# Kernel optimization log

Measured on AMD Instinct MI355X. Metric: run time of the kernel, lower is better.

Reference implementation:

```python
import jax, jax.numpy as jnp
import numpy as np
import math

B, S, D = 4, 4096, 1024
NUM_HEADS = 8  # hardcoded in the original via `// 8` and view(..., 8, head_dim)
HEAD_DIM = D // NUM_HEADS


def setup_inputs() -> dict:
    key = jax.random.key(0)
    ks = jax.random.split(key, 11)
    s = 1.0 / math.sqrt(D)
    inp = {
        "input_seq": jax.random.normal(ks[0], (B, S, D), dtype=jnp.float32),
        # Linear weights stored as [in, out] (y = x @ W + b), matching nn.Linear math
        "Wq": jax.random.uniform(ks[1], (D, D), jnp.float32, -s, s),
        "bq": jax.random.uniform(ks[2], (D,), jnp.float32, -s, s),
        "Wk": jax.random.uniform(ks[3], (D, D), jnp.float32, -s, s),
        "bk": jax.random.uniform(ks[4], (D,), jnp.float32, -s, s),
        "Wv": jax.random.uniform(ks[5], (D, D), jnp.float32, -s, s),
        "bv": jax.random.uniform(ks[6], (D,), jnp.float32, -s, s),
        "W1": jax.random.uniform(ks[7], (D, D), jnp.float32, -s, s),
        "b1": jax.random.uniform(ks[8], (D,), jnp.float32, -s, s),
        "W2": jax.random.uniform(ks[9], (D, D), jnp.float32, -s, s),
        "b2": jax.random.uniform(ks[10], (D,), jnp.float32, -s, s),
    }
    return inp


def reference(input_seq, Wq, bq, Wk, bk, Wv, bv, W1, b1, W2, b2):
    # QKV projections (query=key=input_seq in self-attention)
    q = input_seq @ Wq + bq  # [B,S,D]
    k = input_seq @ Wk + bk
    v = input_seq @ Wv + bv

    # Faithful to the original: view(B, S, 8, head_dim) with NO transpose,
    # so attention is computed over the 8 heads within each token position.
    q = q.reshape(B, S, NUM_HEADS, HEAD_DIM)
    k = k.reshape(B, S, NUM_HEADS, HEAD_DIM)
    v = v.reshape(B, S, NUM_HEADS, HEAD_DIM)

    # scores[b,s,h,t] = q[b,s,h,:] . k[b,s,t,:] / sqrt(head_dim)  -> [B,S,8,8]
    scores = jnp.einsum("bshd,bstd->bsht", q, k) / jnp.sqrt(jnp.float32(HEAD_DIM))
    # dropout on scores before softmax: identity at inference
    attn_weights = jax.nn.softmax(scores, axis=-1)  # [B,S,8,8]

    out = jnp.einsum("bsht,bstd->bshd", attn_weights, v).reshape(B, S, D)
    # dropout on attn_output: identity at inference

    # FFN: Linear -> ReLU -> Linear (no residual / layernorm in the original)
    ff = jnp.maximum(out @ W1 + b1, 0.0) @ W2 + b2
    return ff, attn_weights
```

## Files before the change

### kernel.cpp

```cpp
#include <hip/hip_runtime.h>
#include <hip/hip_bf16.h>


#define DI __device__ __forceinline__

typedef __bf16 bf16raw;
typedef bf16raw bf16x8 __attribute__((ext_vector_type(8)));
typedef float floatx4 __attribute__((ext_vector_type(4)));
typedef unsigned int uint32x4 __attribute__((ext_vector_type(4)));

DI unsigned short f2bf(float f) {
    __hip_bfloat16 h = __float2bfloat16(f);
    return *reinterpret_cast<unsigned short*>(&h);
}

DI void async16(unsigned short* lds, const unsigned short* g) {
    __builtin_amdgcn_global_load_lds(
        (const __attribute__((address_space(1))) void*)g,
        (__attribute__((address_space(3))) void*)lds,
        16, 0, 0);
}

DI unsigned ldsaddr(const void* p) {
    return (unsigned)(unsigned long long)
        (__attribute__((address_space(3))) const void*)p;
}

template <typename T> DI T cvt_out(float v);
template <> DI float cvt_out<float>(float v) { return v; }
template <> DI unsigned short cvt_out<unsigned short>(float v) { return f2bf(v); }

template <int I0, int J0>
DI void mfma16(floatx4 (&acc)[8][4], const uint32x4 (&af)[4][2],
               const uint32x4 (&bf)[2][2]) {
#pragma unroll
    for (int s = 0; s < 2; s++)
#pragma unroll
        for (int i = 0; i < 4; i++)
#pragma unroll
            for (int j = 0; j < 2; j++)
                acc[I0 + i][J0 + j] = __builtin_amdgcn_mfma_f32_16x16x32_bf16(
                    __builtin_bit_cast(bf16x8, af[i][s]),
                    __builtin_bit_cast(bf16x8, bf[j][s]),
                    acc[I0 + i][J0 + j], 0, 0, 0);
}

#define STG_A(b, rb, kt) do { \
    async16(&As[b][(rb) * 64 + wofs], aS + (size_t)(rb) * K + (kt)); \
    async16(&As[b][((rb) + 64) * 64 + wofs], aS + (size_t)((rb) + 64) * K + (kt)); \
} while (0)
#define STG_B(b, rb, kt) do { \
    async16(&Bs[b][(rb) * 64 + wofs], bS + (size_t)(rb) * K + (kt)); \
    async16(&Bs[b][((rb) + 64) * 64 + wofs], bS + (size_t)((rb) + 64) * K + (kt)); \
} while (0)

#define DSR(dst, va, offs) \
    asm volatile("ds_read_b128 %0, %1 offset:" offs : "=&v"(dst) : "v"(va))

#define LDA_LO(dst, va0, va1) do { \
    DSR(dst[0][0], va0, "0");     DSR(dst[0][1], va1, "0"); \
    DSR(dst[1][0], va0, "2048");  DSR(dst[1][1], va1, "2048"); \
    DSR(dst[2][0], va0, "4096");  DSR(dst[2][1], va1, "4096"); \
    DSR(dst[3][0], va0, "6144");  DSR(dst[3][1], va1, "6144"); \
} while (0)
#define LDA_HI(dst, va0, va1) do { \
    DSR(dst[0][0], va0, "16384"); DSR(dst[0][1], va1, "16384"); \
    DSR(dst[1][0], va0, "18432"); DSR(dst[1][1], va1, "18432"); \
    DSR(dst[2][0], va0, "20480"); DSR(dst[2][1], va1, "20480"); \
    DSR(dst[3][0], va0, "22528"); DSR(dst[3][1], va1, "22528"); \
} while (0)
#define LDB_LO(dst, va0, va1) do { \
    DSR(dst[0][0], va0, "0");     DSR(dst[0][1], va1, "0"); \
    DSR(dst[1][0], va0, "2048");  DSR(dst[1][1], va1, "2048"); \
} while (0)
#define LDB_HI(dst, va0, va1) do { \
    DSR(dst[0][0], va0, "16384"); DSR(dst[0][1], va1, "16384"); \
    DSR(dst[1][0], va0, "18432"); DSR(dst[1][1], va1, "18432"); \
} while (0)

#define BARRIER do { __builtin_amdgcn_s_barrier(); \
    __builtin_amdgcn_sched_barrier(0); } while (0)
#define LGKM(n) do { asm volatile("s_waitcnt lgkmcnt(" #n ")" ::: "memory"); \
    __builtin_amdgcn_sched_barrier(0); } while (0)
#define GATE4 asm volatile("s_waitcnt vmcnt(4)" ::: "memory")
#define PRIO1 __builtin_amdgcn_s_setprio(1)
#define PRIO0 __builtin_amdgcn_s_setprio(0)

template <int K, int N, int GX, typename OutT, bool RELU>
__global__ __launch_bounds__(512, 2)
void gemm256_bt(const unsigned short* __restrict__ A,
                const unsigned short* __restrict__ Bt,
                const float* __restrict__ bias,
                OutT* __restrict__ C)
{
    constexpr int BK = 64;
    constexpr int NT = K / BK;
    constexpr int NP = NT / 2;
    static_assert(NT % 2 == 0 && N % 256 == 0, "");

    __shared__ unsigned short As[2][256 * BK];
    __shared__ unsigned short Bs[2][256 * BK];

    const int tid  = threadIdx.x;
    const int wave = tid >> 6;
    const int lane = tid & 63;
    const int quad = lane >> 4;
    const int l16  = lane & 15;
    const int sw7  = l16 & 7;
    const int wm   = wave >> 2;
    const int wn   = wave & 3;

    const int g   = blockIdx.x + GX * blockIdx.y;
    const int xcd = g & 7;
    const int t   = g >> 3;
    const int bx  = t % GX;
    const int by  = t / GX + (gridDim.y >> 3) * xcd;
    const int m0  = by * 256;
    const int n0  = bx * 256;

    const int srow = tid >> 3;
    const int soct = ((tid & 7) ^ (srow & 7)) * 8;
    const unsigned short* aS = A  + (size_t)(m0 + srow) * K + soct;
    const unsigned short* bS = Bt + (size_t)(n0 + srow) * K + soct;
    const int wofs = wave * 512;

    const int aroB = (wm * 64 + l16) * 128;
    const int broB = (wn * 32 + l16) * 128;
    const int s0B  = (quad ^ sw7) * 16;
    const int s1B  = ((quad + 4) ^ sw7) * 16;
    const unsigned vaA0_0 = ldsaddr(&As[0][0]) + aroB + s0B;
    const unsigned vaA0_1 = ldsaddr(&As[0][0]) + aroB + s1B;
    const unsigned vaA1_0 = ldsaddr(&As[1][0]) + aroB + s0B;
    const unsigned vaA1_1 = ldsaddr(&As[1][0]) + aroB + s1B;
    const unsigned vaB0_0 = ldsaddr(&Bs[0][0]) + broB + s0B;
    const unsigned vaB0_1 = ldsaddr(&Bs[0][0]) + broB + s1B;
    const unsigned vaB1_0 = ldsaddr(&Bs[1][0]) + broB + s0B;
    const unsigned vaB1_1 = ldsaddr(&Bs[1][0]) + broB + s1B;

    floatx4 acc[8][4];
    const floatx4 zero = {0.f, 0.f, 0.f, 0.f};
#pragma unroll
    for (int i = 0; i < 8; i++)
#pragma unroll
        for (int j = 0; j < 4; j++) acc[i][j] = zero;

    uint32x4 aL[4][2], aH[4][2], bL[2][2], bH[2][2];

    STG_A(0, 0, 0); STG_B(0, 0, 0); STG_B(0, 128, 0); STG_A(0, 128, 0);
    STG_A(1, 0, BK); STG_B(1, 0, BK); STG_B(1, 128, BK); STG_A(1, 128, BK);
    asm volatile("s_waitcnt vmcnt(8)" ::: "memory");
    BARRIER;
    LDA_LO(aL, vaA0_0, vaA0_1);
    LDB_LO(bL, vaB0_0, vaB0_1);
    LGKM(0);

#pragma unroll 1
    for (int it = 0; it < NP; ++it) {
        const int kt2 = ((2 * it + 2) < NT ? (2 * it + 2) : (NT - 1)) * BK;
        const int kt3 = ((2 * it + 3) < NT ? (2 * it + 3) : (NT - 1)) * BK;

        BARRIER;
        LDB_HI(bH, vaB0_0, vaB0_1);
        STG_A(0, 0, kt2);
        LGKM(4);
        PRIO1; mfma16<0, 0>(acc, aL, bL); PRIO0;

        BARRIER;
        LDA_HI(aH, vaA0_0, vaA0_1);
        STG_B(0, 0, kt2);
        LGKM(8);
        PRIO1; mfma16<0, 2>(acc, aL, bH); PRIO0;

        GATE4;
        BARRIER;
        LDA_LO(aL, vaA1_0, vaA1_1);
        STG_B(0, 128, kt2);
        LGKM(8);
        PRIO1; mfma16<4, 0>(acc, aH, bL); PRIO0;

        BARRIER;
        LDB_LO(bL, vaB1_0, vaB1_1);
        STG_A(0, 128, kt2);
        LGKM(4);
        PRIO1; mfma16<4, 2>(acc, aH, bH); PRIO0;

        BARRIER;
        LDB_HI(bH, vaB1_0, vaB1_1);
        STG_A(1, 0, kt3);
        LGKM(4);
        PRIO1; mfma16<0, 0>(acc, aL, bL); PRIO0;

        BARRIER;
        LDA_HI(aH, vaA1_0, vaA1_1);
        STG_B(1, 0, kt3);
        LGKM(8);
        PRIO1; mfma16<0, 2>(acc, aL, bH); PRIO0;

        GATE4;
        BARRIER;
        LDA_LO(aL, vaA0_0, vaA0_1);
        STG_B(1, 128, kt3);
        LGKM(8);
        PRIO1; mfma16<4, 0>(acc, aH, bL); PRIO0;

        BARRIER;
        LDB_LO(bL, vaB0_0, vaB0_1);
        STG_A(1, 128, kt3);
        LGKM(4);
        PRIO1; mfma16<4, 2>(acc, aH, bH); PRIO0;
    }
    asm volatile("s_waitcnt vmcnt(0) lgkmcnt(0)" ::: "memory");
    __builtin_amdgcn_sched_barrier(0);

#pragma unroll
    for (int j = 0; j < 4; j++) {
        const int col = n0 + wn * 32 + (j & 1) * 16 + (j >> 1) * 128 + l16;
        const float bv = bias[col];
#pragma unroll
        for (int i = 0; i < 8; i++) {
            const int rb = m0 + wm * 64 + (i & 3) * 16 + (i >> 2) * 128 + quad * 4;
#pragma unroll
            for (int r = 0; r < 4; r++) {
                float v = acc[i][j][r] + bv;
                if (RELU) v = fmaxf(v, 0.f);
                C[(size_t)(rb + r) * N + col] = cvt_out<OutT>(v);
            }
        }
    }
}

#undef STG_A
#undef STG_B
#undef DSR
#undef LDA_LO
#undef LDA_HI
#undef LDB_LO
#undef LDB_HI
#undef BARRIER
#undef LGKM
#undef GATE4
#undef PRIO1
#undef PRIO0

__global__ void cast_f32_to_bf16(const float* __restrict__ src,
                                 unsigned short* __restrict__ dst, int n4) {
    int i = blockIdx.x * blockDim.x + threadIdx.x;
    if (i < n4) {
        float4 v = reinterpret_cast<const float4*>(src)[i];
        ushort4 o = { f2bf(v.x), f2bf(v.y), f2bf(v.z), f2bf(v.w) };
        reinterpret_cast<ushort4*>(dst)[i] = o;
    }
}

struct WPack {
    const float* src[5];
    unsigned short* dst[5];
};
__global__ void transpose_cast_all(WPack p) {
    __shared__ float tile[32][33];
    const float* W = p.src[blockIdx.z];
    unsigned short* Wt = p.dst[blockIdx.z];
    const int n0 = blockIdx.x * 32, k0 = blockIdx.y * 32;
    const int tx = threadIdx.x, ty = threadIdx.y;
#pragma unroll
    for (int i = 0; i < 32; i += 8)
        tile[ty + i][tx] = W[(size_t)(k0 + ty + i) * 1024 + n0 + tx];
    __syncthreads();
#pragma unroll
    for (int i = 0; i < 32; i += 8)
        Wt[(size_t)(n0 + ty + i) * 1024 + k0 + tx] = f2bf(tile[tx][ty + i]);
}

__global__ void concat_bias(const float* __restrict__ bq,
                            const float* __restrict__ bk,
                            const float* __restrict__ bv,
                            float* __restrict__ dst) {
    int i = blockIdx.x * blockDim.x + threadIdx.x;
    const float* s = (i < 1024) ? bq : ((i < 2048) ? bk : bv);
    dst[i] = s[i & 1023];
}

DI float dot8(unsigned a, unsigned b, float acc) {
    union { unsigned u; float f; } al, ah, bl, bh;
    al.u = a << 16; ah.u = a & 0xffff0000u;
    bl.u = b << 16; bh.u = b & 0xffff0000u;
    return acc + al.f * bl.f + ah.f * bh.f;
}

__global__ __launch_bounds__(256)
void attention_kernel(const unsigned short* __restrict__ qkv,
                      unsigned short* __restrict__ out_bf,
                      float* __restrict__ attn_w)
{
    __shared__ unsigned short sqkv[4][3072];
    __shared__ float sw[4][64];
    const int tid  = threadIdx.x;
    const int wave = tid >> 6;
    const int lane = tid & 63;
    const int m    = blockIdx.x * 4 + wave;

    {
        const uint4* src = reinterpret_cast<const uint4*>(qkv + (size_t)m * 3072);
        uint4* dst = reinterpret_cast<uint4*>(&sqkv[wave][0]);
#pragma unroll
        for (int i = 0; i < 6; i++) dst[lane + 64 * i] = src[lane + 64 * i];
    }
    __syncthreads();

    {
        const int h = lane >> 3, t = lane & 7;
        const uint2* q8 = reinterpret_cast<const uint2*>(&sqkv[wave][h * 128]);
        const uint2* k8 = reinterpret_cast<const uint2*>(&sqkv[wave][1024 + t * 128]);
        float dot = 0.f;
#pragma unroll
        for (int d = 0; d < 32; d++) {
            uint2 a = q8[d], b = k8[d];
            dot = dot8(a.x, b.x, dot);
            dot = dot8(a.y, b.y, dot);
        }
        float score = dot * 0.08838834764831843f;
        float mx = score;
#pragma unroll
        for (int o = 1; o < 8; o <<= 1) mx = fmaxf(mx, __shfl_xor(mx, o, 8));
        float e = __expf(score - mx);
        float sum = e;
#pragma unroll
        for (int o = 1; o < 8; o <<= 1) sum += __shfl_xor(sum, o, 8);
        float w = e / sum;
        sw[wave][lane] = w;
        attn_w[(size_t)m * 64 + lane] = w;
    }
    __syncthreads();

    {
        const int h  = lane >> 3;
        const int d0 = (lane & 7) * 16;
        float acc[16];
#pragma unroll
        for (int i = 0; i < 16; i++) acc[i] = 0.f;
#pragma unroll
        for (int t = 0; t < 8; t++) {
            const float w = sw[wave][h * 8 + t];
            const uint4* v8 = reinterpret_cast<const uint4*>(
                &sqkv[wave][2048 + t * 128 + d0]);
            uint4 v0 = v8[0], v1 = v8[1];
            unsigned vv[8] = { v0.x, v0.y, v0.z, v0.w, v1.x, v1.y, v1.z, v1.w };
#pragma unroll
            for (int i = 0; i < 8; i++) {
                union { unsigned u; float f; } lo, hi;
                lo.u = vv[i] << 16; hi.u = vv[i] & 0xffff0000u;
                acc[i * 2]     += w * lo.f;
                acc[i * 2 + 1] += w * hi.f;
            }
        }
        unsigned o[8];
#pragma unroll
        for (int i = 0; i < 8; i++)
            o[i] = (unsigned)f2bf(acc[i * 2]) | ((unsigned)f2bf(acc[i * 2 + 1]) << 16);
        uint4* dst = reinterpret_cast<uint4*>(out_bf + (size_t)m * 1024 + lane * 16);
        dst[0] = make_uint4(o[0], o[1], o[2], o[3]);
        dst[1] = make_uint4(o[4], o[5], o[6], o[7]);
    }
}

extern "C" void kernel_launch(void* const* d_in, const int* in_sizes, int n_in,
                              void* d_out, int out_size, void* d_ws, size_t ws_size,
                              hipStream_t stream) {
    const float* x  = (const float*)d_in[0];
    const float* Wq = (const float*)d_in[1];
    const float* bq = (const float*)d_in[2];
    const float* Wk = (const float*)d_in[3];
    const float* bk = (const float*)d_in[4];
    const float* Wv = (const float*)d_in[5];
    const float* bv = (const float*)d_in[6];
    const float* W1 = (const float*)d_in[7];
    const float* b1 = (const float*)d_in[8];
    const float* W2 = (const float*)d_in[9];
    const float* b2 = (const float*)d_in[10];

    constexpr int D = 1024;
    constexpr int M = 4 * 4096;
    constexpr size_t XN = (size_t)M * D;

    float* ff_out   = (float*)d_out;
    float* attn_out = (float*)d_out + XN;

    char* ws = (char*)d_ws;
    size_t off = 0;
    auto alloc = [&](size_t bytes) -> char* {
        char* p = ws + off;
        off += (bytes + 255) & ~(size_t)255;
        return p;
    };
    unsigned short* Xbf   = (unsigned short*)alloc(XN * 2);
    unsigned short* Wtqkv = (unsigned short*)alloc((size_t)3 * D * D * 2);
    unsigned short* Wt1   = (unsigned short*)alloc((size_t)D * D * 2);
    unsigned short* Wt2   = (unsigned short*)alloc((size_t)D * D * 2);
    float*          bqkv  = (float*)alloc(3 * D * 4);
    unsigned short* outbf = (unsigned short*)alloc(XN * 2);
    unsigned short* hbf   = (unsigned short*)alloc(XN * 2);
    unsigned short* qkv   = (unsigned short*)alloc((size_t)M * 3 * D * 2);

    cast_f32_to_bf16<<<(int)(XN / 4 / 256), 256, 0, stream>>>(x, Xbf, (int)(XN / 4));
    WPack p;
    p.src[0] = Wq; p.dst[0] = Wtqkv;
    p.src[1] = Wk; p.dst[1] = Wtqkv + (size_t)D * D;
    p.src[2] = Wv; p.dst[2] = Wtqkv + (size_t)2 * D * D;
    p.src[3] = W1; p.dst[3] = Wt1;
    p.src[4] = W2; p.dst[4] = Wt2;
    transpose_cast_all<<<dim3(32, 32, 5), dim3(32, 8), 0, stream>>>(p);
    concat_bias<<<12, 256, 0, stream>>>(bq, bk, bv, bqkv);

    gemm256_bt<D, 3 * D, 12, unsigned short, false>
        <<<dim3(12, 64), 512, 0, stream>>>(Xbf, Wtqkv, bqkv, qkv);
    attention_kernel<<<M / 4, 256, 0, stream>>>(qkv, outbf, attn_out);

    gemm256_bt<D, D, 4, unsigned short, true>
        <<<dim3(4, 64), 512, 0, stream>>>(outbf, Wt1, b1, hbf);
    gemm256_bt<D, D, 4, float, false>
        <<<dim3(4, 64), 512, 0, stream>>>(hbf, Wt2, b2, ff_out);
}
```

Before: 364.2 us.

## Restructure GEMM main loop with two barriers per phase and full LDS waits

Rewrites the software pipeline of the 256x256 bf16 GEMM main loop. Each phase now issues an LDS fragment read plus one global-to-LDS stage, waits for all LDS reads before its MFMA block, and then gates on vmcnt(12) with a second barrier. The earlier partial lgkmcnt waits and the single vmcnt(4) gate per half are gone, and stage issue order and the prologue change with them. The aim is a more regular hazard-safe schedule, but doubling the barriers and using full lgkm waits may cut the overlap between memory traffic and MFMA work.

After: 371.6 us. 1.02x slower.

```diff
diff --git a/kernel.cpp b/kernel.cpp
--- a/kernel.cpp
+++ b/kernel.cpp
@@ -78,11 +78,10 @@
     DSR(dst[1][0], va0, "18432"); DSR(dst[1][1], va1, "18432"); \
 } while (0)
 
-#define BARRIER do { __builtin_amdgcn_s_barrier(); \
-    __builtin_amdgcn_sched_barrier(0); } while (0)
-#define LGKM(n) do { asm volatile("s_waitcnt lgkmcnt(" #n ")" ::: "memory"); \
-    __builtin_amdgcn_sched_barrier(0); } while (0)
-#define GATE4 asm volatile("s_waitcnt vmcnt(4)" ::: "memory")
+#define SBAR __builtin_amdgcn_sched_barrier(0)
+#define BAR do { __builtin_amdgcn_s_barrier(); SBAR; } while (0)
+#define LGKM0 do { asm volatile("s_waitcnt lgkmcnt(0)" ::: "memory"); SBAR; } while (0)
+#define GATE12 do { asm volatile("s_waitcnt vmcnt(12)" ::: "memory"); SBAR; } while (0)
 #define PRIO1 __builtin_amdgcn_s_setprio(1)
 #define PRIO0 __builtin_amdgcn_s_setprio(0)
 
@@ -96,7 +95,7 @@
     constexpr int BK = 64;
     constexpr int NT = K / BK;
     constexpr int NP = NT / 2;
-    static_assert(NT % 2 == 0 && N % 256 == 0, "");
+    static_assert(NT % 2 == 0 && NT >= 4 && N % 256 == 0, "");
 
     __shared__ unsigned short As[2][256 * BK];
     __shared__ unsigned short Bs[2][256 * BK];
@@ -146,71 +145,69 @@
 
     uint32x4 aL[4][2], aH[4][2], bL[2][2], bH[2][2];
 
-    STG_A(0, 0, 0); STG_B(0, 0, 0); STG_B(0, 128, 0); STG_A(0, 128, 0);
-    STG_A(1, 0, BK); STG_B(1, 0, BK); STG_B(1, 128, BK); STG_A(1, 128, BK);
-    asm volatile("s_waitcnt vmcnt(8)" ::: "memory");
-    BARRIER;
-    LDA_LO(aL, vaA0_0, vaA0_1);
+    STG_B(0, 0, 0);  STG_A(0, 0, 0);  STG_B(0, 128, 0);  STG_A(0, 128, 0);
+    STG_B(1, 0, BK); STG_A(1, 0, BK); STG_B(1, 128, BK); STG_A(1, 128, BK);
+    GATE12;
+    BAR;
     LDB_LO(bL, vaB0_0, vaB0_1);
-    LGKM(0);
+    LGKM0;
+    BAR;
 
 #pragma unroll 1
     for (int it = 0; it < NP; ++it) {
         const int kt2 = ((2 * it + 2) < NT ? (2 * it + 2) : (NT - 1)) * BK;
         const int kt3 = ((2 * it + 3) < NT ? (2 * it + 3) : (NT - 1)) * BK;
 
-        BARRIER;
+        LDA_LO(aL, vaA0_0, vaA0_1);
+        STG_B(0, 0, kt2);
+        SBAR; BAR; LGKM0;
+        PRIO1; mfma16<0, 0>(acc, aL, bL); PRIO0;
+        GATE12; BAR;
+
         LDB_HI(bH, vaB0_0, vaB0_1);
         STG_A(0, 0, kt2);
-        LGKM(4);
-        PRIO1; mfma16<0, 0>(acc, aL, bL); PRIO0;
-
-        BARRIER;
+        SBAR; BAR; LGKM0;
+        PRIO1; mfma16<0, 2>(acc, aL, bH); PRIO0;
+        GATE12; BAR;
+
         LDA_HI(aH, vaA0_0, vaA0_1);
-        STG_B(0, 0, kt2);
-        LGKM(8);
-        PRIO1; mfma16<0, 2>(acc, aL, bH); PRIO0;
-
-        GATE4;
-        BARRIER;
-        LDA_LO(aL, vaA1_0, vaA1_1);
         STG_B(0, 128, kt2);
-        LGKM(8);
+        SBAR; BAR; LGKM0;
         PRIO1; mfma16<4, 0>(acc, aH, bL); PRIO0;
-
-        BARRIER;
+        GATE12; BAR;
+
         LDB_LO(bL, vaB1_0, vaB1_1);
         STG_A(0, 128, kt2);
-        LGKM(4);
+        SBAR; BAR; LGKM0;
         PRIO1; mfma16<4, 2>(acc, aH, bH); PRIO0;
-
-        BARRIER;
+        GATE12; BAR;
+
+        LDA_LO(aL, vaA1_0, vaA1_1);
+        STG_B(1, 0, kt3);
+        SBAR; BAR; LGKM0;
+        PRIO1; mfma16<0, 0>(acc, aL, bL); PRIO0;
+        GATE12; BAR;
+
         LDB_HI(bH, vaB1_0, vaB1_1);
         STG_A(1, 0, kt3);
-        LGKM(4);
-        PRIO1; mfma16<0, 0>(acc, aL, bL); PRIO0;
-
-        BARRIER;
+        SBAR; BAR; LGKM0;
+        PRIO1; mfma16<0, 2>(acc, aL, bH); PRIO0;
+        GATE12; BAR;
+
         LDA_HI(aH, vaA1_0, vaA1_1);
-        STG_B(1, 0, kt3);
-        LGKM(8);
-        PRIO1; mfma16<0, 2>(acc, aL, bH); PRIO0;
-
-        GATE4;
-        BARRIER;
-        LDA_LO(aL, vaA0_0, vaA0_1);
         STG_B(1, 128, kt3);
-        LGKM(8);
+        SBAR; BAR; LGKM0;
         PRIO1; mfma16<4, 0>(acc, aH, bL); PRIO0;
-
-        BARRIER;
+        GATE12; BAR;
+
         LDB_LO(bL, vaB0_0, vaB0_1);
         STG_A(1, 128, kt3);
-        LGKM(4);
+        SBAR; BAR; LGKM0;
         PRIO1; mfma16<4, 2>(acc, aH, bH); PRIO0;
+        GATE12; BAR;
     }
     asm volatile("s_waitcnt vmcnt(0) lgkmcnt(0)" ::: "memory");
-    __builtin_amdgcn_sched_barrier(0);
+    SBAR;
 
 #pragma unroll
     for (int j = 0; j < 4; j++) {
@@ -236,9 +233,10 @@
 #undef LDA_HI
 #undef LDB_LO
 #undef LDB_HI
-#undef BARRIER
-#undef LGKM
-#undef GATE4
+#undef SBAR
+#undef BAR
+#undef LGKM0
+#undef GATE12
 #undef PRIO1
 #undef PRIO0
 
```
